# Optimization experiments

Measured on AMD Instinct MI355X. Metric: run time of the kernel, lower is better.

Reference implementation:

```python
import jax, jax.numpy as jnp
import numpy as np


def _gcn_conv(x, W, b, src, dst, num_nodes):
    # x: [N, F_in], W: [F_in, F_out], b: [F_out]
    # src/dst already include self-loops. Symmetric normalization per PyG GCNConv.
    ones = jnp.ones(src.shape[0], dtype=x.dtype)
    deg = jax.ops.segment_sum(ones, dst, num_segments=num_nodes)  # in-degree w/ self-loops
    dinv = jnp.where(deg > 0, jax.lax.rsqrt(deg), 0.0)
    norm = dinv[src] * dinv[dst]                                  # [E]
    h = x @ W                                                     # [N, F_out]
    msg = h[src] * norm[:, None]                                  # gather + scale
    out = jax.ops.segment_sum(msg, dst, num_segments=num_nodes)   # scatter-add
    return out + b


def setup_inputs() -> dict:
    key = jax.random.key(0)
    k1, k2, k3, k4, k5, k6 = jax.random.split(key, 6)
    N, E = 1000000, 4000000
    x = jax.random.normal(k1, (N, 4), dtype=jnp.float32)
    edge_index = jax.random.randint(k2, (2, E), 0, N, dtype=jnp.int64)
    W1 = jax.random.normal(k3, (4, 16), dtype=jnp.float32) * 0.5
    b1 = jax.random.normal(k4, (16,), dtype=jnp.float32) * 0.1
    W2 = jax.random.normal(k5, (16, 2), dtype=jnp.float32) * 0.25
    b2 = jax.random.normal(k6, (2,), dtype=jnp.float32) * 0.1
    return {"x": x, "edge_index": edge_index, "num_nodes": N,
            "W1": W1, "b1": b1, "W2": W2, "b2": b2}


def reference(x, edge_index, num_nodes, W1, b1, W2, b2):
    # Add self-loops once (GCNConv default add_self_loops=True)
    loop = jnp.arange(num_nodes, dtype=edge_index.dtype)
    src = jnp.concatenate([edge_index[0], loop])
    dst = jnp.concatenate([edge_index[1], loop])
    h = jax.nn.relu(_gcn_conv(x, W1, b1, src, dst, num_nodes))
    h = _gcn_conv(h, W2, b2, src, dst, num_nodes)
    return jax.nn.log_softmax(h, axis=1)
```

## Files before the change

kernel.cpp:

```cpp
#include <hip/hip_runtime.h>


typedef unsigned int u32;

#define BSHIFT 11
#define BNODES 2048
#define MAXNB 512
#define EPB 16384

__global__ void k_bincount(const int* __restrict__ dst, int E, int NB,
                           u32* __restrict__ bucketTotal) {
    __shared__ u32 h[MAXNB];
    const int tid = threadIdx.x;
    for (int j = tid; j < MAXNB; j += 256) h[j] = 0;
    __syncthreads();
    const int start = blockIdx.x * EPB;
    const int end = min(start + EPB, E);
    for (int e = start + tid; e < end; e += 256)
        atomicAdd(&h[((u32)dst[e]) >> BSHIFT], 1u);
    __syncthreads();
    for (int j = tid; j < NB; j += 256)
        if (h[j]) atomicAdd(&bucketTotal[j], h[j]);
}

__global__ void k_bucketscan(const u32* __restrict__ bucketTotal,
                             u32* __restrict__ bucketBase,
                             u32* __restrict__ cursor, int NB, int E) {
    __shared__ u32 s[MAXNB];
    const int tid = threadIdx.x;
    u32 v = (tid < NB) ? bucketTotal[tid] : 0u;
    s[tid] = v;
    __syncthreads();
    for (int d = 1; d < MAXNB; d <<= 1) {
        u32 t = (tid >= d) ? s[tid - d] : 0u;
        __syncthreads();
        s[tid] += t;
        __syncthreads();
    }
    u32 excl = s[tid] - v;
    if (tid < NB) { bucketBase[tid] = excl; cursor[tid] = excl; }
    if (tid == 0) bucketBase[NB] = (u32)E;
}

__global__ void k_binscatter(const int* __restrict__ src, const int* __restrict__ dst,
                             int E, int NB, u32* __restrict__ cursor,
                             u32* __restrict__ rec) {
    __shared__ u32 h[MAXNB];
    const int tid = threadIdx.x;
    for (int j = tid; j < MAXNB; j += 256) h[j] = 0;
    __syncthreads();
    const int start = blockIdx.x * EPB;
    const int end = min(start + EPB, E);
    for (int e = start + tid; e < end; e += 256)
        atomicAdd(&h[((u32)dst[e]) >> BSHIFT], 1u);
    __syncthreads();
    for (int j = tid; j < NB; j += 256) {
        u32 c = h[j];
        h[j] = c ? atomicAdd(&cursor[j], c) : 0u;
    }
    __syncthreads();
    for (int e = start + tid; e < end; e += 256) {
        u32 d = (u32)dst[e];
        u32 b = d >> BSHIFT;
        u32 slot = atomicAdd(&h[b], 1u);
        rec[slot] = ((u32)src[e]) | ((d & (BNODES - 1u)) << 20);
    }
}

__global__ void k_deg(const u32* __restrict__ rec, const u32* __restrict__ bucketBase,
                      float* __restrict__ dinv, int N) {
    __shared__ u32 deg[BNODES];
    const int tid = threadIdx.x;
    const int b = blockIdx.x;
    for (int j = tid; j < BNODES; j += 256) deg[j] = 0;
    __syncthreads();
    const u32 s0 = bucketBase[b], s1 = bucketBase[b + 1];
    for (u32 i = s0 + tid; i < s1; i += 256)
        atomicAdd(&deg[rec[i] >> 20], 1u);
    __syncthreads();
    const int nodeBase = b << BSHIFT;
    for (int n = tid; n < BNODES; n += 256) {
        int gn = nodeBase + n;
        if (gn < N) dinv[gn] = rsqrtf((float)(deg[n] + 1u));
    }
}

__global__ void k_l1(const u32* __restrict__ rec, const u32* __restrict__ bucketBase,
                     const float* __restrict__ dinv, const float4* __restrict__ x,
                     const float* __restrict__ W1, const float* __restrict__ b1,
                     const float* __restrict__ W2,
                     float2* __restrict__ h2d, int N) {
    __shared__ float agg[BNODES * 4];
    const int tid = threadIdx.x;
    const int b = blockIdx.x;
    for (int j = tid; j < BNODES * 4; j += 1024) agg[j] = 0.f;
    __syncthreads();
    const u32 s0 = bucketBase[b], s1 = bucketBase[b + 1];
    for (u32 i = s0 + tid; i < s1; i += 1024) {
        u32 r = rec[i];
        u32 s = r & 0xFFFFFu;
        u32 dl = r >> 20;
        float ds = dinv[s];
        float4 v = x[s];
        atomicAdd(&agg[dl * 4 + 0], v.x * ds);
        atomicAdd(&agg[dl * 4 + 1], v.y * ds);
        atomicAdd(&agg[dl * 4 + 2], v.z * ds);
        atomicAdd(&agg[dl * 4 + 3], v.w * ds);
    }
    __syncthreads();
    const int nodeBase = b << BSHIFT;
    for (int n = tid; n < BNODES; n += 1024) {
        int gn = nodeBase + n;
        if (gn >= N) continue;
        float di = dinv[gn];
        float4 xi = x[gn];
        float ax = (xi.x * di + agg[n * 4 + 0]) * di;
        float ay = (xi.y * di + agg[n * 4 + 1]) * di;
        float az = (xi.z * di + agg[n * 4 + 2]) * di;
        float aw = (xi.w * di + agg[n * 4 + 3]) * di;
        float g0 = 0.f, g1 = 0.f;
#pragma unroll
        for (int k = 0; k < 16; ++k) {
            float h = ax * W1[k] + ay * W1[16 + k] + az * W1[32 + k] + aw * W1[48 + k] + b1[k];
            h = fmaxf(h, 0.f);
            g0 += h * W2[2 * k];
            g1 += h * W2[2 * k + 1];
        }
        h2d[gn] = make_float2(g0 * di, g1 * di);
    }
}

__global__ void k_l2(const u32* __restrict__ rec, const u32* __restrict__ bucketBase,
                     const float* __restrict__ dinv, const float2* __restrict__ h2d,
                     const float* __restrict__ b2, float2* __restrict__ out, int N) {
    __shared__ float agg[BNODES * 2];
    const int tid = threadIdx.x;
    const int b = blockIdx.x;
    for (int j = tid; j < BNODES * 2; j += 1024) agg[j] = 0.f;
    __syncthreads();
    const u32 s0 = bucketBase[b], s1 = bucketBase[b + 1];
    for (u32 i = s0 + tid; i < s1; i += 1024) {
        u32 r = rec[i];
        u32 s = r & 0xFFFFFu;
        u32 dl = r >> 20;
        float2 v = h2d[s];
        atomicAdd(&agg[dl * 2 + 0], v.x);
        atomicAdd(&agg[dl * 2 + 1], v.y);
    }
    __syncthreads();
    const int nodeBase = b << BSHIFT;
    for (int n = tid; n < BNODES; n += 1024) {
        int gn = nodeBase + n;
        if (gn >= N) continue;
        float di = dinv[gn];
        float2 self = h2d[gn];
        float g0 = (self.x + agg[n * 2 + 0]) * di + b2[0];
        float g1 = (self.y + agg[n * 2 + 1]) * di + b2[1];
        float m = fmaxf(g0, g1);
        float l = m + logf(expf(g0 - m) + expf(g1 - m));
        out[gn] = make_float2(g0 - l, g1 - l);
    }
}

extern "C" void kernel_launch(void* const* d_in, const int* in_sizes, int n_in,
                              void* d_out, int out_size, void* d_ws, size_t ws_size,
                              hipStream_t stream) {
    const float* x  = (const float*)d_in[0];
    const int*   ei = (const int*)d_in[1];
    const float* W1 = (const float*)d_in[3];
    const float* b1 = (const float*)d_in[4];
    const float* W2 = (const float*)d_in[5];
    const float* b2 = (const float*)d_in[6];

    const int N = in_sizes[0] / 4;
    const int E = in_sizes[1] / 2;
    const int* src = ei;
    const int* dst = ei + E;
    const int NB = (N + BNODES - 1) >> BSHIFT;

    char* w = (char*)d_ws;
    u32*    rec  = (u32*)(w);
    float*  dinv = (float*)(w + 4 * (size_t)E);
    float2* h2d  = (float2*)(w + 4 * (size_t)E + 4 * (size_t)N);
    u32*    bucketTotal = (u32*)(w + 4 * (size_t)E + 12 * (size_t)N);
    u32*    bucketBase  = bucketTotal + MAXNB;
    u32*    cursor      = bucketBase + MAXNB + 1;

    const int gA = (E + EPB - 1) / EPB;

    hipMemsetAsync(bucketTotal, 0, sizeof(u32) * (size_t)NB, stream);
    k_bincount<<<gA, 256, 0, stream>>>(dst, E, NB, bucketTotal);
    k_bucketscan<<<1, MAXNB, 0, stream>>>(bucketTotal, bucketBase, cursor, NB, E);
    k_binscatter<<<gA, 256, 0, stream>>>(src, dst, E, NB, cursor, rec);
    k_deg<<<NB, 256, 0, stream>>>(rec, bucketBase, dinv, N);
    k_l1<<<NB, 1024, 0, stream>>>(rec, bucketBase, dinv, (const float4*)x, W1, b1, W2, h2d, N);
    k_l2<<<NB, 1024, 0, stream>>>(rec, bucketBase, dinv, h2d, b2, (float2*)d_out, N);
}
```

Measured before the change: 332.3 us.

## Store per-block bucket histograms, prescale features in bf16, and unroll edge loops

k_bincount now saves each block's bucket histogram, so k_binscatter no longer re-reads dst to recount. k_deg now writes x*dinv as packed bf16, which removes the dinv gather in layer 1 and halves the gathered bytes. The layer-2 intermediate is also stored as packed bf16. Both aggregation loops are unrolled by two and k_deg uses 512 threads. The bf16 storage cuts random-gather traffic but lowers precision of the aggregated features, which risks accuracy tolerance.

```diff
diff --git a/kernel.cpp b/kernel.cpp
--- a/kernel.cpp
+++ b/kernel.cpp
@@ -8,8 +8,17 @@
 #define MAXNB 512
 #define EPB 16384
 
+__device__ __forceinline__ u32 pack_bf16(float a, float b) {
+    u32 ua = __float_as_uint(a), ub = __float_as_uint(b);
+    ua += 0x7FFFu + ((ua >> 16) & 1u);
+    ub += 0x7FFFu + ((ub >> 16) & 1u);
+    return (ua >> 16) | (ub & 0xFFFF0000u);
+}
+__device__ __forceinline__ float bf_lo(u32 p) { return __uint_as_float(p << 16); }
+__device__ __forceinline__ float bf_hi(u32 p) { return __uint_as_float(p & 0xFFFF0000u); }
+
 __global__ void k_bincount(const int* __restrict__ dst, int E, int NB,
-                           u32* __restrict__ bucketTotal) {
+                           u32* __restrict__ bucketTotal, u32* __restrict__ bh) {
     __shared__ u32 h[MAXNB];
     const int tid = threadIdx.x;
     for (int j = tid; j < MAXNB; j += 256) h[j] = 0;
@@ -19,8 +28,12 @@
     for (int e = start + tid; e < end; e += 256)
         atomicAdd(&h[((u32)dst[e]) >> BSHIFT], 1u);
     __syncthreads();
-    for (int j = tid; j < NB; j += 256)
-        if (h[j]) atomicAdd(&bucketTotal[j], h[j]);
+    u32* bhrow = bh + (size_t)blockIdx.x * MAXNB;
+    for (int j = tid; j < NB; j += 256) {
+        u32 c = h[j];
+        bhrow[j] = c;
+        if (c) atomicAdd(&bucketTotal[j], c);
+    }
 }
 
 __global__ void k_bucketscan(const u32* __restrict__ bucketTotal,
@@ -44,21 +57,19 @@
 
 __global__ void k_binscatter(const int* __restrict__ src, const int* __restrict__ dst,
                              int E, int NB, u32* __restrict__ cursor,
-                             u32* __restrict__ rec) {
+                             const u32* __restrict__ bh, u32* __restrict__ rec) {
     __shared__ u32 h[MAXNB];
     const int tid = threadIdx.x;
+    const u32* bhrow = bh + (size_t)blockIdx.x * MAXNB;
     for (int j = tid; j < MAXNB; j += 256) h[j] = 0;
+    __syncthreads();
+    for (int j = tid; j < NB; j += 256) {
+        u32 c = bhrow[j];
+        if (c) h[j] = atomicAdd(&cursor[j], c);
+    }
     __syncthreads();
     const int start = blockIdx.x * EPB;
     const int end = min(start + EPB, E);
-    for (int e = start + tid; e < end; e += 256)
-        atomicAdd(&h[((u32)dst[e]) >> BSHIFT], 1u);
-    __syncthreads();
-    for (int j = tid; j < NB; j += 256) {
-        u32 c = h[j];
-        h[j] = c ? atomicAdd(&cursor[j], c) : 0u;
-    }
-    __syncthreads();
     for (int e = start + tid; e < end; e += 256) {
         u32 d = (u32)dst[e];
         u32 b = d >> BSHIFT;
@@ -68,56 +79,69 @@
 }
 
 __global__ void k_deg(const u32* __restrict__ rec, const u32* __restrict__ bucketBase,
-                      float* __restrict__ dinv, int N) {
+                      const float4* __restrict__ x,
+                      float* __restrict__ dinv, uint2* __restrict__ xd, int N) {
     __shared__ u32 deg[BNODES];
     const int tid = threadIdx.x;
     const int b = blockIdx.x;
-    for (int j = tid; j < BNODES; j += 256) deg[j] = 0;
+    for (int j = tid; j < BNODES; j += 512) deg[j] = 0;
     __syncthreads();
     const u32 s0 = bucketBase[b], s1 = bucketBase[b + 1];
-    for (u32 i = s0 + tid; i < s1; i += 256)
+    for (u32 i = s0 + tid; i < s1; i += 512)
         atomicAdd(&deg[rec[i] >> 20], 1u);
     __syncthreads();
     const int nodeBase = b << BSHIFT;
-    for (int n = tid; n < BNODES; n += 256) {
+    for (int n = tid; n < BNODES; n += 512) {
         int gn = nodeBase + n;
-        if (gn < N) dinv[gn] = rsqrtf((float)(deg[n] + 1u));
+        if (gn < N) {
+            float d = rsqrtf((float)(deg[n] + 1u));
+            dinv[gn] = d;
+            float4 xi = x[gn];
+            xd[gn] = make_uint2(pack_bf16(xi.x * d, xi.y * d),
+                                pack_bf16(xi.z * d, xi.w * d));
+        }
     }
 }
 
 __global__ void k_l1(const u32* __restrict__ rec, const u32* __restrict__ bucketBase,
-                     const float* __restrict__ dinv, const float4* __restrict__ x,
+                     const float* __restrict__ dinv, const uint2* __restrict__ xd,
                      const float* __restrict__ W1, const float* __restrict__ b1,
                      const float* __restrict__ W2,
-                     float2* __restrict__ h2d, int N) {
+                     u32* __restrict__ h2, int N) {
     __shared__ float agg[BNODES * 4];
     const int tid = threadIdx.x;
     const int b = blockIdx.x;
     for (int j = tid; j < BNODES * 4; j += 1024) agg[j] = 0.f;
     __syncthreads();
     const u32 s0 = bucketBase[b], s1 = bucketBase[b + 1];
-    for (u32 i = s0 + tid; i < s1; i += 1024) {
-        u32 r = rec[i];
-        u32 s = r & 0xFFFFFu;
-        u32 dl = r >> 20;
-        float ds = dinv[s];
-        float4 v = x[s];
-        atomicAdd(&agg[dl * 4 + 0], v.x * ds);
-        atomicAdd(&agg[dl * 4 + 1], v.y * ds);
-        atomicAdd(&agg[dl * 4 + 2], v.z * ds);
-        atomicAdd(&agg[dl * 4 + 3], v.w * ds);
-    }
-    __syncthreads();
+
+#define L1_EDGE(I) do {                                   \
+        u32 r = rec[I];                                   \
+        u32 s = r & 0xFFFFFu;                             \
+        float* p = &agg[(r >> 20) * 4];                   \
+        uint2 v = xd[s];                                  \
+        atomicAdd(p + 0, bf_lo(v.x));                     \
+        atomicAdd(p + 1, bf_hi(v.x));                     \
+        atomicAdd(p + 2, bf_lo(v.y));                     \
+        atomicAdd(p + 3, bf_hi(v.y));                     \
+    } while (0)
+
+    u32 i = s0 + tid;
+    for (; i + 1024 < s1; i += 2048) { L1_EDGE(i); L1_EDGE(i + 1024); }
+    if (i < s1) L1_EDGE(i);
+#undef L1_EDGE
+    __syncthreads();
+
     const int nodeBase = b << BSHIFT;
     for (int n = tid; n < BNODES; n += 1024) {
         int gn = nodeBase + n;
         if (gn >= N) continue;
         float di = dinv[gn];
-        float4 xi = x[gn];
-        float ax = (xi.x * di + agg[n * 4 + 0]) * di;
-        float ay = (xi.y * di + agg[n * 4 + 1]) * di;
-        float az = (xi.z * di + agg[n * 4 + 2]) * di;
-        float aw = (xi.w * di + agg[n * 4 + 3]) * di;
+        uint2 xs = xd[gn];
+        float ax = (bf_lo(xs.x) + agg[n * 4 + 0]) * di;
+        float ay = (bf_hi(xs.x) + agg[n * 4 + 1]) * di;
+        float az = (bf_lo(xs.y) + agg[n * 4 + 2]) * di;
+        float aw = (bf_hi(xs.y) + agg[n * 4 + 3]) * di;
         float g0 = 0.f, g1 = 0.f;
 #pragma unroll
         for (int k = 0; k < 16; ++k) {
@@ -126,12 +150,12 @@
             g0 += h * W2[2 * k];
             g1 += h * W2[2 * k + 1];
         }
-        h2d[gn] = make_float2(g0 * di, g1 * di);
+        h2[gn] = pack_bf16(g0 * di, g1 * di);
     }
 }
 
 __global__ void k_l2(const u32* __restrict__ rec, const u32* __restrict__ bucketBase,
-                     const float* __restrict__ dinv, const float2* __restrict__ h2d,
+                     const float* __restrict__ dinv, const u32* __restrict__ h2,
                      const float* __restrict__ b2, float2* __restrict__ out, int N) {
     __shared__ float agg[BNODES * 2];
     const int tid = threadIdx.x;
@@ -139,23 +163,30 @@
     for (int j = tid; j < BNODES * 2; j += 1024) agg[j] = 0.f;
     __syncthreads();
     const u32 s0 = bucketBase[b], s1 = bucketBase[b + 1];
-    for (u32 i = s0 + tid; i < s1; i += 1024) {
-        u32 r = rec[i];
-        u32 s = r & 0xFFFFFu;
-        u32 dl = r >> 20;
-        float2 v = h2d[s];
-        atomicAdd(&agg[dl * 2 + 0], v.x);
-        atomicAdd(&agg[dl * 2 + 1], v.y);
-    }
-    __syncthreads();
+
+#define L2_EDGE(I) do {                                   \
+        u32 r = rec[I];                                   \
+        u32 s = r & 0xFFFFFu;                             \
+        float* p = &agg[(r >> 20) * 2];                   \
+        u32 v = h2[s];                                    \
+        atomicAdd(p + 0, bf_lo(v));                       \
+        atomicAdd(p + 1, bf_hi(v));                       \
+    } while (0)
+
+    u32 i = s0 + tid;
+    for (; i + 1024 < s1; i += 2048) { L2_EDGE(i); L2_EDGE(i + 1024); }
+    if (i < s1) L2_EDGE(i);
+#undef L2_EDGE
+    __syncthreads();
+
     const int nodeBase = b << BSHIFT;
     for (int n = tid; n < BNODES; n += 1024) {
         int gn = nodeBase + n;
         if (gn >= N) continue;
         float di = dinv[gn];
-        float2 self = h2d[gn];
-        float g0 = (self.x + agg[n * 2 + 0]) * di + b2[0];
-        float g1 = (self.y + agg[n * 2 + 1]) * di + b2[1];
+        u32 self = h2[gn];
+        float g0 = (bf_lo(self) + agg[n * 2 + 0]) * di + b2[0];
+        float g1 = (bf_hi(self) + agg[n * 2 + 1]) * di + b2[1];
         float m = fmaxf(g0, g1);
         float l = m + logf(expf(g0 - m) + expf(g1 - m));
         out[gn] = make_float2(g0 - l, g1 - l);
@@ -177,22 +208,24 @@
     const int* src = ei;
     const int* dst = ei + E;
     const int NB = (N + BNODES - 1) >> BSHIFT;
+    const int gA = (E + EPB - 1) / EPB;
 
     char* w = (char*)d_ws;
-    u32*    rec  = (u32*)(w);
-    float*  dinv = (float*)(w + 4 * (size_t)E);
-    float2* h2d  = (float2*)(w + 4 * (size_t)E + 4 * (size_t)N);
-    u32*    bucketTotal = (u32*)(w + 4 * (size_t)E + 12 * (size_t)N);
-    u32*    bucketBase  = bucketTotal + MAXNB;
-    u32*    cursor      = bucketBase + MAXNB + 1;
-
-    const int gA = (E + EPB - 1) / EPB;
+    u32*   rec  = (u32*)(w);
+    float* dinv = (float*)(w + 4 * (size_t)E);
+    uint2* xd   = (uint2*)(w + 4 * (size_t)E + 4 * (size_t)N);
+    u32*   h2   = (u32*)(w + 4 * (size_t)E + 12 * (size_t)N);
+    u32*   meta = (u32*)(w + 4 * (size_t)E + 16 * (size_t)N);
+    u32*   bucketTotal = meta;
+    u32*   bucketBase  = meta + MAXNB;
+    u32*   cursor      = meta + MAXNB + MAXNB + 1;
+    u32*   bh          = meta + 3 * MAXNB + 2;
 
     hipMemsetAsync(bucketTotal, 0, sizeof(u32) * (size_t)NB, stream);
-    k_bincount<<<gA, 256, 0, stream>>>(dst, E, NB, bucketTotal);
+    k_bincount<<<gA, 256, 0, stream>>>(dst, E, NB, bucketTotal, bh);
     k_bucketscan<<<1, MAXNB, 0, stream>>>(bucketTotal, bucketBase, cursor, NB, E);
-    k_binscatter<<<gA, 256, 0, stream>>>(src, dst, E, NB, cursor, rec);
-    k_deg<<<NB, 256, 0, stream>>>(rec, bucketBase, dinv, N);
-    k_l1<<<NB, 1024, 0, stream>>>(rec, bucketBase, dinv, (const float4*)x, W1, b1, W2, h2d, N);
-    k_l2<<<NB, 1024, 0, stream>>>(rec, bucketBase, dinv, h2d, b2, (float2*)d_out, N);
-}
+    k_binscatter<<<gA, 256, 0, stream>>>(src, dst, E, NB, cursor, bh, rec);
+    k_deg<<<NB, 512, 0, stream>>>(rec, bucketBase, (const float4*)x, dinv, xd, N);
+    k_l1<<<NB, 1024, 0, stream>>>(rec, bucketBase, dinv, xd, W1, b1, W2, h2, N);
+    k_l2<<<NB, 1024, 0, stream>>>(rec, bucketBase, dinv, h2, b2, (float2*)d_out, N);
+}
```

Result: no change. 332.2 us (-0.0%).
